# Optimization experiments

Measured on AMD Instinct MI355X. Metric: run time of the kernel, lower is better.

## Reference

```python
import jax, jax.numpy as jnp
import numpy as np

B, S, D = 256, 70, 128
NUM_NODE = 40000
N_SAMPLE = 12
ALPHA = 0.2  # leaky-relu slope


def setup_inputs() -> dict:
    key = jax.random.key(0)
    ks = jax.random.split(key, 16)
    stdv = 1.0 / np.sqrt(D)
    u = lambda k, shp: jax.random.uniform(k, shp, jnp.float32, -stdv, stdv)
    inputs = jax.random.randint(ks[0], (B, S), 0, NUM_NODE)
    adj = jax.random.randint(ks[1], (B, S, S), 0, 5)
    mask_item = jnp.ones((B, S), jnp.int32)
    item = jax.random.randint(ks[2], (B, S), 0, NUM_NODE)
    input_times = jax.random.uniform(ks[3], (B, S), jnp.float32)
    adj_all = jax.random.randint(ks[4], (NUM_NODE, N_SAMPLE), 0, NUM_NODE)
    num_w = jax.random.uniform(ks[5], (NUM_NODE, N_SAMPLE), jnp.float32)
    embedding = u(ks[6], (NUM_NODE, D))
    a0, a1, a2, a3 = (u(ks[7 + i], (D,)) for i in range(4))
    gw1 = u(ks[11], (D + 1, D))
    gw2 = u(ks[12], (D, 1))
    gw3 = u(ks[13], (2 * D, D))
    gbias = u(ks[14], (D,))
    return dict(inputs=inputs, adj=adj, mask_item=mask_item, item=item,
                input_times=input_times, adj_all=adj_all, num_w=num_w,
                embedding=embedding, a0=a0, a1=a1, a2=a2, a3=a3,
                gw1=gw1, gw2=gw2, gw3=gw3, gbias=gbias)


def reference(inputs, adj, mask_item, item, input_times, adj_all, num_w,
              embedding, a0, a1, a2, a3, gw1, gw2, gw3, gbias):
    # ---- local aggregator (4-relation GAT over session graph) ----
    h = embedding[inputs]                              # [B,S,D]
    a_in = h[:, :, None, :] * h[:, None, :, :]         # [B,S,S,D] pairwise products
    att = lambda a: jax.nn.leaky_relu(jnp.einsum('bijd,d->bij', a_in, a), ALPHA)
    e0, e1, e2, e3 = att(a0), att(a1), att(a2), att(a3)
    neg = jnp.full_like(e0, -9e15)
    alpha = jnp.where(adj == 1, e0, neg)
    alpha = jnp.where(adj == 2, e1, alpha)
    alpha = jnp.where(adj == 3, e2, alpha)
    alpha = jnp.where(adj == 4, e3, alpha)
    alpha = jax.nn.softmax(alpha, axis=-1)
    h_local = jnp.einsum('bij,bjd->bid', alpha, h)     # [B,S,D]

    # ---- global aggregator: 1-hop neighbor sampling + session-gated attention ----
    flat = inputs.reshape(-1)
    neigh = adj_all[flat].reshape(B, S, N_SAMPLE)      # sampled neighbor ids
    nw = num_w[flat].reshape(B, S, N_SAMPLE)           # neighbor co-occurrence weights
    nv = embedding[neigh]                              # [B,S,K,D]

    maskf = mask_item.astype(jnp.float32)[..., None]   # [B,S,1]
    item_emb = embedding[item] * maskf
    sess = jnp.sum(item_emb, axis=1) / jnp.sum(maskf, axis=1)   # [B,D] mean session emb
    extra = sess[:, None, None, :]                     # broadcast to [B,S,K,D]

    feat = jnp.concatenate([extra * nv, nw[..., None]], axis=-1)  # [B,S,K,D+1]
    al = jax.nn.leaky_relu(feat @ gw1, 0.2)            # [B,S,K,D]
    al = jax.nn.softmax((al @ gw2)[..., 0], axis=-1)[..., None]   # [B,S,K,1]
    nagg = jnp.sum(al * nv, axis=-2)                   # [B,S,D]

    out = jnp.concatenate([h, nagg], axis=-1) @ gw3 + gbias
    h_global = jax.nn.relu(out)                        # [B,S,D]
    # dropout_local/global = 0 (eval mode): identity
    return h_local, h_global
```

## Files before the change

kernel.cpp:

```cpp
#include <hip/hip_runtime.h>
#include <hip/hip_bf16.h>

#define B_ 256
#define S_ 70
#define D_ 128
#define NSAMP 12
#define NNODE 40000
#define HGLOB (B_ * S_ * D_)
#define IBLK 14
#define NPOS 10
#define NR2 (NPOS * NSAMP)
#define NRP 128

typedef float  f32x4 __attribute__((ext_vector_type(4)));
typedef short  s16x8 __attribute__((ext_vector_type(8)));

__device__ __forceinline__ unsigned short f2bf(float x) {
    union { float f; unsigned u; } v; v.f = x;
    return (unsigned short)((v.u + 0x7FFF + ((v.u >> 16) & 1)) >> 16);
}
__device__ __forceinline__ float bf2f(unsigned short u) {
    union { unsigned u; float f; } v; v.u = ((unsigned)u) << 16;
    return v.f;
}

__global__ __launch_bounds__(512) void prelude_kernel(const int* __restrict__ item,
                                                      const int* __restrict__ mask,
                                                      const float* __restrict__ emb,
                                                      const float* __restrict__ gw1,
                                                      const float* __restrict__ gw3,
                                                      float* __restrict__ sess,
                                                      unsigned short* __restrict__ gw1T,
                                                      unsigned short* __restrict__ gw3T,
                                                      unsigned short* __restrict__ embT) {
    if (blockIdx.x < B_) {
        __shared__ float pacc[4][D_];
        __shared__ float pm[4];
        int b = blockIdx.x;
        int d = threadIdx.x & 127, q = threadIdx.x >> 7;
        float acc = 0.f, msum = 0.f;
        for (int s = q; s < S_; s += 4) {
            int node = item[b * S_ + s];
            float m = (float)mask[b * S_ + s];
            acc += m * emb[(long)node * D_ + d];
            msum += m;
        }
        pacc[q][d] = acc;
        if (d == 0) pm[q] = msum;
        __syncthreads();
        if (q == 0) {
            float a = pacc[0][d] + pacc[1][d] + pacc[2][d] + pacc[3][d];
            float m = pm[0] + pm[1] + pm[2] + pm[3];
            sess[b * D_ + d] = a / m;
        }
    } else if (blockIdx.x < B_ + 96) {
        int idx = (blockIdx.x - B_) * 512 + threadIdx.x;
        if (idx < 128 * 128) {
            int c = idx >> 7, r = idx & 127;
            gw1T[idx] = f2bf(gw1[r * 128 + c]);
        } else if (idx < 128 * 128 + 128 * 256) {
            int j = idx - 128 * 128;
            int c = j >> 8, r = j & 255;
            gw3T[j] = f2bf(gw3[r * 128 + c]);
        }
    } else {
        long idx = (long)(blockIdx.x - (B_ + 96)) * 512 + threadIdx.x;
        if (idx < (long)NNODE * D_ / 8) {
            const float4* src = (const float4*)(emb + idx * 8);
            float4 e0 = src[0], e1 = src[1];
            s16x8 p;
            p[0] = (short)f2bf(e0.x); p[1] = (short)f2bf(e0.y);
            p[2] = (short)f2bf(e0.z); p[3] = (short)f2bf(e0.w);
            p[4] = (short)f2bf(e1.x); p[5] = (short)f2bf(e1.y);
            p[6] = (short)f2bf(e1.z); p[7] = (short)f2bf(e1.w);
            *(s16x8*)(embT + idx * 8) = p;
        }
    }
}

struct LocalSM {
    unsigned short hl[72 * 128];
    float          El[16 * 84];
    unsigned short al[16 * 104];
    int            ids[72];
};
struct GlobalSM {
    unsigned short nv[NRP * 128];
    unsigned short cat[16 * 256];
    float          spart[NRP][4];
    int            neigh[NR2];
    float          nw[NR2];
    float          score[NR2];
    float          wsm[NR2];
};

union FusedSM { LocalSM loc; GlobalSM glob; };

__global__ __launch_bounds__(256) void fused_kernel(
        const int* __restrict__ inputs, const int* __restrict__ adj,
        const int* __restrict__ adj_all, const float* __restrict__ num_w,
        const unsigned short* __restrict__ embT, const float* __restrict__ sess,
        const float* __restrict__ a0p, const float* __restrict__ a1p,
        const float* __restrict__ a2p, const float* __restrict__ a3p,
        const unsigned short* __restrict__ gw1T, const float* __restrict__ gw1,
        const float* __restrict__ gw2,
        const unsigned short* __restrict__ gw3T, const float* __restrict__ gbias,
        float* __restrict__ out) {
    __shared__ __align__(16) FusedSM smem;

    const int L = blockIdx.x;
    const int b = L / 12;
    const int r = L - b * 12;
    const int tid  = threadIdx.x;
    const int lane = tid & 63, wave = tid >> 6;
    const int l15  = lane & 15, l4 = lane >> 4;
    const s16x8 zero8 = {0, 0, 0, 0, 0, 0, 0, 0};

    if (r < 5) {
        LocalSM* P = &smem.loc;
        const int i0 = r * IBLK;

        if (tid < S_) P->ids[tid] = inputs[b * S_ + tid];
        if (tid < 32) ((s16x8*)P->hl)[70 * 16 + tid] = zero8;
        __syncthreads();

        #pragma unroll
        for (int it = 0; it < 5; ++it) {
            int idx = it * 256 + tid;
            if (idx < S_ * 16) {
                int s = idx >> 4, c8 = idx & 15;
                s16x8 p = *(const s16x8*)(embT + (long)P->ids[s] * D_ + c8 * 8);
                ((s16x8*)P->hl)[s * 16 + (c8 ^ (s & 7))] = p;
            }
        }
        __syncthreads();

        s16x8 af_all[4][4];
        {
            const float* aptr[4] = {a0p, a1p, a2p, a3p};
            int hrow = i0 + l15;
            #pragma unroll
            for (int ks = 0; ks < 4; ++ks) {
                s16x8 hf = ((s16x8*)P->hl)[hrow * 16 + ((ks * 4 + l4) ^ (hrow & 7))];
                #pragma unroll
                for (int rr = 0; rr < 4; ++rr) {
                    const float* ar = aptr[rr];
                    float4 alo = *(const float4*)(ar + ks * 32 + l4 * 8);
                    float4 ahi = *(const float4*)(ar + ks * 32 + l4 * 8 + 4);
                    s16x8 o;
                    o[0] = (short)f2bf(bf2f((unsigned short)hf[0]) * alo.x);
                    o[1] = (short)f2bf(bf2f((unsigned short)hf[1]) * alo.y);
                    o[2] = (short)f2bf(bf2f((unsigned short)hf[2]) * alo.z);
                    o[3] = (short)f2bf(bf2f((unsigned short)hf[3]) * alo.w);
                    o[4] = (short)f2bf(bf2f((unsigned short)hf[4]) * ahi.x);
                    o[5] = (short)f2bf(bf2f((unsigned short)hf[5]) * ahi.y);
                    o[6] = (short)f2bf(bf2f((unsigned short)hf[6]) * ahi.z);
                    o[7] = (short)f2bf(bf2f((unsigned short)hf[7]) * ahi.w);
                    af_all[rr][ks] = o;
                }
            }
        }

        for (int n = wave; n < 5; n += 4) {
            s16x8 bfr[4];
            int jr = n * 16 + l15;
            int jrc = jr < 72 ? jr : 71;
            #pragma unroll
            for (int ks = 0; ks < 4; ++ks)
                bfr[ks] = ((s16x8*)P->hl)[jrc * 16 + ((ks * 4 + l4) ^ (jrc & 7))];

            f32x4 ac0 = {0.f,0.f,0.f,0.f}, ac1 = {0.f,0.f,0.f,0.f};
            f32x4 ac2 = {0.f,0.f,0.f,0.f}, ac3 = {0.f,0.f,0.f,0.f};
            #pragma unroll
            for (int ks = 0; ks < 4; ++ks) {
                ac0 = __builtin_amdgcn_mfma_f32_16x16x32_bf16(af_all[0][ks], bfr[ks], ac0, 0, 0, 0);
                ac1 = __builtin_amdgcn_mfma_f32_16x16x32_bf16(af_all[1][ks], bfr[ks], ac1, 0, 0, 0);
                ac2 = __builtin_amdgcn_mfma_f32_16x16x32_bf16(af_all[2][ks], bfr[ks], ac2, 0, 0, 0);
                ac3 = __builtin_amdgcn_mfma_f32_16x16x32_bf16(af_all[3][ks], bfr[ks], ac3, 0, 0, 0);
            }

            #pragma unroll
            for (int reg = 0; reg < 4; ++reg) {
                int il = l4 * 4 + reg;
                int i  = i0 + il;
                int j  = n * 16 + l15;
                float v;
                if (j < S_) {
                    int ic = i < S_ ? i : S_ - 1;
                    int a  = adj[((long)b * S_ + ic) * S_ + j];
                    float raw = (a == 1) ? ac0[reg] : (a == 2) ? ac1[reg]
                              : (a == 3) ? ac2[reg] : (a == 4) ? ac3[reg] : 0.f;
                    v = (a >= 1 && a <= 4) ? (raw > 0.f ? raw : 0.2f * raw) : -9e15f;
                } else {
                    v = -INFINITY;
                }
                P->El[il * 84 + j] = v;
            }
        }
        __syncthreads();

        {
            int g = tid >> 4, li = tid & 15;
            float mx = -INFINITY;
            for (int j = li; j < S_; j += 16) mx = fmaxf(mx, P->El[g * 84 + j]);
            #pragma unroll
            for (int o = 1; o < 16; o <<= 1) mx = fmaxf(mx, __shfl_xor(mx, o));
            float sm = 0.f;
            for (int j = li; j < S_; j += 16) {
                float ex = __expf(P->El[g * 84 + j] - mx);
                P->El[g * 84 + j] = ex;
                sm += ex;
            }
            #pragma unroll
            for (int o = 1; o < 16; o <<= 1) sm += __shfl_xor(sm, o);
            float inv = 1.f / sm;
            for (int j = li; j < 104; j += 16)
                P->al[g * 104 + j] = (j < S_) ? f2bf(P->El[g * 84 + j] * inv) : (unsigned short)0;
        }
        __syncthreads();

        for (int n = wave; n < 8; n += 4) {
            f32x4 acc = {0.f, 0.f, 0.f, 0.f};
            int d = n * 16 + l15;
            int dchunk = d >> 3, de = d & 7;
            #pragma unroll
            for (int ks = 0; ks < 3; ++ks) {
                s16x8 afp = *(const s16x8*)(P->al + l15 * 104 + ks * 32 + l4 * 8);
                int jb = ks * 32 + l4 * 8;
                s16x8 bfp;
                #pragma unroll
                for (int e = 0; e < 8; ++e) {
                    int j = jb + e;
                    bfp[e] = (j < 72)
                        ? (short)P->hl[j * 128 + ((dchunk ^ (j & 7)) << 3) + de]
                        : (short)0;
                }
                acc = __builtin_amdgcn_mfma_f32_16x16x32_bf16(afp, bfp, acc, 0, 0, 0);
            }
            #pragma unroll
            for (int reg = 0; reg < 4; ++reg) {
                int il = l4 * 4 + reg;
                if (il < IBLK)
                    out[((long)b * S_ + (i0 + il)) * D_ + d] = acc[reg];
            }
        }
    } else {
        GlobalSM* P = &smem.glob;
        const int i0  = (r - 5) * NPOS;
        const int bs0 = b * S_ + i0;

        if (tid < NR2) {
            int p = tid / NSAMP;
            int k = tid - p * NSAMP;
            int node = inputs[bs0 + p];
            P->neigh[tid] = adj_all[node * NSAMP + k];
            P->nw[tid]    = num_w[node * NSAMP + k];
        }
        if (tid < 128) ((s16x8*)P->nv)[NR2 * 16 + tid] = zero8;
        __syncthreads();

        #pragma unroll
        for (int it = 0; it < 8; ++it) {
            int idx = it * 256 + tid;
            if (idx < NR2 * 16) {
                int row = idx >> 4, c8 = idx & 15;
                s16x8 p = *(const s16x8*)(embT + (long)P->neigh[row] * D_ + c8 * 8);
                ((s16x8*)P->nv)[row * 16 + (c8 ^ (row & 7))] = p;
            }
        }
        __syncthreads();

        s16x8 bfp[2][4];
        #pragma unroll
        for (int n = 0; n < 2; ++n) {
            int c = (wave * 2 + n) * 16 + l15;
            #pragma unroll
            for (int ks = 0; ks < 4; ++ks) {
                s16x8 g = *(const s16x8*)(gw1T + c * 128 + ks * 32 + l4 * 8);
                float4 slo = *(const float4*)(sess + b * D_ + ks * 32 + l4 * 8);
                float4 shi = *(const float4*)(sess + b * D_ + ks * 32 + l4 * 8 + 4);
                s16x8 o;
                o[0] = (short)f2bf(bf2f((unsigned short)g[0]) * slo.x);
                o[1] = (short)f2bf(bf2f((unsigned short)g[1]) * slo.y);
                o[2] = (short)f2bf(bf2f((unsigned short)g[2]) * slo.z);
                o[3] = (short)f2bf(bf2f((unsigned short)g[3]) * slo.w);
                o[4] = (short)f2bf(bf2f((unsigned short)g[4]) * shi.x);
                o[5] = (short)f2bf(bf2f((unsigned short)g[5]) * shi.y);
                o[6] = (short)f2bf(bf2f((unsigned short)g[6]) * shi.z);
                o[7] = (short)f2bf(bf2f((unsigned short)g[7]) * shi.w);
                bfp[n][ks] = o;
            }
        }
        float g128a = gw1[128 * 128 + wave * 32 + l15];
        float g128b = gw1[128 * 128 + wave * 32 + 16 + l15];
        float gw2a  = gw2[wave * 32 + l15];
        float gw2b  = gw2[wave * 32 + 16 + l15];

        for (int m = 0; m < NRP / 16; ++m) {
            int arow = m * 16 + l15;
            s16x8 af[4];
            #pragma unroll
            for (int ks = 0; ks < 4; ++ks)
                af[ks] = ((s16x8*)P->nv)[arow * 16 + ((ks * 4 + l4) ^ (arow & 7))];

            f32x4 acc0 = {0.f, 0.f, 0.f, 0.f}, acc1 = {0.f, 0.f, 0.f, 0.f};
            #pragma unroll
            for (int ks = 0; ks < 4; ++ks) {
                acc0 = __builtin_amdgcn_mfma_f32_16x16x32_bf16(af[ks], bfp[0][ks], acc0, 0, 0, 0);
                acc1 = __builtin_amdgcn_mfma_f32_16x16x32_bf16(af[ks], bfp[1][ks], acc1, 0, 0, 0);
            }

            float sp[4];
            #pragma unroll
            for (int reg = 0; reg < 4; ++reg) {
                int rr = m * 16 + l4 * 4 + reg;
                float nwv = (rr < NR2) ? P->nw[rr] : 0.f;
                float al0 = acc0[reg] + nwv * g128a;
                float al1 = acc1[reg] + nwv * g128b;
                al0 = al0 > 0.f ? al0 : 0.2f * al0;
                al1 = al1 > 0.f ? al1 : 0.2f * al1;
                sp[reg] = al0 * gw2a + al1 * gw2b;
            }
            #pragma unroll
            for (int off = 1; off < 16; off <<= 1) {
                #pragma unroll
                for (int reg = 0; reg < 4; ++reg) sp[reg] += __shfl_xor(sp[reg], off);
            }
            if (l15 == 0) {
                int rb = m * 16 + l4 * 4;
                #pragma unroll
                for (int reg = 0; reg < 4; ++reg) P->spart[rb + reg][wave] = sp[reg];
            }
        }
        __syncthreads();

        if (tid < NR2)
            P->score[tid] = P->spart[tid][0] + P->spart[tid][1] + P->spart[tid][2] + P->spart[tid][3];
        __syncthreads();

        if (tid < NPOS) {
            float mx = -1e30f;
            #pragma unroll
            for (int k = 0; k < NSAMP; ++k) mx = fmaxf(mx, P->score[tid * NSAMP + k]);
            float ex[NSAMP]; float ss = 0.f;
            #pragma unroll
            for (int k = 0; k < NSAMP; ++k) { ex[k] = __expf(P->score[tid * NSAMP + k] - mx); ss += ex[k]; }
            float inv = 1.f / ss;
            #pragma unroll
            for (int k = 0; k < NSAMP; ++k) P->wsm[tid * NSAMP + k] = ex[k] * inv;
        }
        __syncthreads();

        {
            int p  = tid >> 4;
            int c8 = tid & 15;
            if (p < NPOS) {
                float a0v[4] = {0.f,0.f,0.f,0.f}, a1v[4] = {0.f,0.f,0.f,0.f};
                #pragma unroll
                for (int k = 0; k < NSAMP; ++k) {
                    int row = p * NSAMP + k;
                    float w = P->wsm[row];
                    s16x8 nvv = ((s16x8*)P->nv)[row * 16 + (c8 ^ (row & 7))];
                    a0v[0] += w * bf2f((unsigned short)nvv[0]);
                    a0v[1] += w * bf2f((unsigned short)nvv[1]);
                    a0v[2] += w * bf2f((unsigned short)nvv[2]);
                    a0v[3] += w * bf2f((unsigned short)nvv[3]);
                    a1v[0] += w * bf2f((unsigned short)nvv[4]);
                    a1v[1] += w * bf2f((unsigned short)nvv[5]);
                    a1v[2] += w * bf2f((unsigned short)nvv[6]);
                    a1v[3] += w * bf2f((unsigned short)nvv[7]);
                }
                int node = inputs[bs0 + p];
                s16x8 ph = *(const s16x8*)(embT + (long)node * D_ + c8 * 8);
                s16x8 pa;
                pa[0]=(short)f2bf(a0v[0]); pa[1]=(short)f2bf(a0v[1]); pa[2]=(short)f2bf(a0v[2]); pa[3]=(short)f2bf(a0v[3]);
                pa[4]=(short)f2bf(a1v[0]); pa[5]=(short)f2bf(a1v[1]); pa[6]=(short)f2bf(a1v[2]); pa[7]=(short)f2bf(a1v[3]);
                ((s16x8*)P->cat)[p * 32 + ( c8       ^ (p & 7))] = ph;
                ((s16x8*)P->cat)[p * 32 + ((16 + c8) ^ (p & 7))] = pa;
            } else {
                ((s16x8*)P->cat)[p * 32 + ( c8       ^ (p & 7))] = zero8;
                ((s16x8*)P->cat)[p * 32 + ((16 + c8) ^ (p & 7))] = zero8;
            }
        }
        __syncthreads();

        {
            f32x4 acc0 = {0.f,0.f,0.f,0.f}, acc1 = {0.f,0.f,0.f,0.f};
            int arow = l15;
            int cc = wave * 32 + l15;
            #pragma unroll
            for (int ks = 0; ks < 8; ++ks) {
                s16x8 a  = ((s16x8*)P->cat)[arow * 32 + ((ks * 4 + l4) ^ (arow & 7))];
                s16x8 b0 = *(const s16x8*)(gw3T +  cc       * 256 + ks * 32 + l4 * 8);
                s16x8 b1 = *(const s16x8*)(gw3T + (cc + 16) * 256 + ks * 32 + l4 * 8);
                acc0 = __builtin_amdgcn_mfma_f32_16x16x32_bf16(a, b0, acc0, 0, 0, 0);
                acc1 = __builtin_amdgcn_mfma_f32_16x16x32_bf16(a, b1, acc1, 0, 0, 0);
            }
            float gb0 = gbias[wave * 32 + l15];
            float gb1 = gbias[wave * 32 + 16 + l15];
            #pragma unroll
            for (int reg = 0; reg < 4; ++reg) {
                int il = l4 * 4 + reg;
                if (il < NPOS) {
                    long bs = bs0 + il;
                    float o0 = acc0[reg] + gb0;
                    float o1 = acc1[reg] + gb1;
                    out[(long)HGLOB + bs * D_ + wave * 32 + l15]      = o0 > 0.f ? o0 : 0.f;
                    out[(long)HGLOB + bs * D_ + wave * 32 + 16 + l15] = o1 > 0.f ? o1 : 0.f;
                }
            }
        }
    }
}

extern "C" void kernel_launch(void* const* d_in, const int* in_sizes, int n_in,
                              void* d_out, int out_size, void* d_ws, size_t ws_size,
                              hipStream_t stream) {
    const int*   inputs  = (const int*)  d_in[0];
    const int*   adj     = (const int*)  d_in[1];
    const int*   mask    = (const int*)  d_in[2];
    const int*   item    = (const int*)  d_in[3];
    const int*   adj_all = (const int*)  d_in[5];
    const float* num_w   = (const float*)d_in[6];
    const float* emb     = (const float*)d_in[7];
    const float* a0      = (const float*)d_in[8];
    const float* a1      = (const float*)d_in[9];
    const float* a2      = (const float*)d_in[10];
    const float* a3      = (const float*)d_in[11];
    const float* gw1     = (const float*)d_in[12];
    const float* gw2     = (const float*)d_in[13];
    const float* gw3     = (const float*)d_in[14];
    const float* gbias   = (const float*)d_in[15];
    float* out = (float*)d_out;

    float*          sess = (float*)d_ws;
    unsigned short* gw1T = (unsigned short*)((char*)d_ws + 131072);
    unsigned short* gw3T = gw1T + 128 * 128;
    unsigned short* embT = gw3T + 128 * 256;

    const int embt_blocks = (NNODE * D_ / 8 + 511) / 512;
    prelude_kernel<<<B_ + 96 + embt_blocks, 512, 0, stream>>>(item, mask, emb, gw1, gw3,
                                                              sess, gw1T, gw3T, embT);
    fused_kernel<<<B_ * 12, 256, 0, stream>>>(inputs, adj, adj_all, num_w, embT, sess,
                                              a0, a1, a2, a3,
                                              gw1T, gw1, gw2, gw3T, gbias, out);
}
```

Baseline: 80.49 us.

## Add transposed LDS copy of session embeddings and pack 12 positions per global block

The local blocks now also write a transposed bf16 copy of the gathered session embeddings into LDS, so the alpha·h MFMA B-operand becomes one vector load instead of eight scalar gathers. The global path now handles 12 positions per block instead of 10, which cuts the block count from 12 to 11 per session and removes the padding rows and bounds checks from the neighbour tile. The costs are a larger local LDS footprint (zero-fill plus scattered 2-byte transposed writes, which may cause bank conflicts) and some clamped duplicate work in the last global block.

Measured after the change: 87.30 us. +8.5%, slower.

```diff
diff --git a/kernel.cpp b/kernel.cpp
--- a/kernel.cpp
+++ b/kernel.cpp
@@ -8,9 +8,10 @@
 #define NNODE 40000
 #define HGLOB (B_ * S_ * D_)
 #define IBLK 14
-#define NPOS 10
+#define NPOS 12
 #define NR2 (NPOS * NSAMP)
-#define NRP 128
+#define NROLE (5 + 6)
+#define HTS 72
 
 typedef float  f32x4 __attribute__((ext_vector_type(4)));
 typedef short  s16x8 __attribute__((ext_vector_type(8)));
@@ -80,14 +81,15 @@
 
 struct LocalSM {
     unsigned short hl[72 * 128];
+    unsigned short HT[128 * HTS + 96];
     float          El[16 * 84];
     unsigned short al[16 * 104];
     int            ids[72];
 };
 struct GlobalSM {
-    unsigned short nv[NRP * 128];
+    unsigned short nv[NR2 * 128];
     unsigned short cat[16 * 256];
-    float          spart[NRP][4];
+    float          spart[NR2][4];
     int            neigh[NR2];
     float          nw[NR2];
     float          score[NR2];
@@ -109,8 +111,8 @@
     __shared__ __align__(16) FusedSM smem;
 
     const int L = blockIdx.x;
-    const int b = L / 12;
-    const int r = L - b * 12;
+    const int b = L / NROLE;
+    const int r = L - b * NROLE;
     const int tid  = threadIdx.x;
     const int lane = tid & 63, wave = tid >> 6;
     const int l15  = lane & 15, l4 = lane >> 4;
@@ -122,6 +124,7 @@
 
         if (tid < S_) P->ids[tid] = inputs[b * S_ + tid];
         if (tid < 32) ((s16x8*)P->hl)[70 * 16 + tid] = zero8;
+        for (int c = tid; c < (128 * HTS + 96) / 8; c += 256) ((s16x8*)P->HT)[c] = zero8;
         __syncthreads();
 
         #pragma unroll
@@ -131,6 +134,9 @@
                 int s = idx >> 4, c8 = idx & 15;
                 s16x8 p = *(const s16x8*)(embT + (long)P->ids[s] * D_ + c8 * 8);
                 ((s16x8*)P->hl)[s * 16 + (c8 ^ (s & 7))] = p;
+                #pragma unroll
+                for (int e = 0; e < 8; ++e)
+                    P->HT[(c8 * 8 + e) * HTS + s] = (unsigned short)p[e];
             }
         }
         __syncthreads();
@@ -222,19 +228,10 @@
         for (int n = wave; n < 8; n += 4) {
             f32x4 acc = {0.f, 0.f, 0.f, 0.f};
             int d = n * 16 + l15;
-            int dchunk = d >> 3, de = d & 7;
             #pragma unroll
             for (int ks = 0; ks < 3; ++ks) {
                 s16x8 afp = *(const s16x8*)(P->al + l15 * 104 + ks * 32 + l4 * 8);
-                int jb = ks * 32 + l4 * 8;
-                s16x8 bfp;
-                #pragma unroll
-                for (int e = 0; e < 8; ++e) {
-                    int j = jb + e;
-                    bfp[e] = (j < 72)
-                        ? (short)P->hl[j * 128 + ((dchunk ^ (j & 7)) << 3) + de]
-                        : (short)0;
-                }
+                s16x8 bfp = *(const s16x8*)(P->HT + d * HTS + ks * 32 + l4 * 8);
                 acc = __builtin_amdgcn_mfma_f32_16x16x32_bf16(afp, bfp, acc, 0, 0, 0);
             }
             #pragma unroll
@@ -252,21 +249,19 @@
         if (tid < NR2) {
             int p = tid / NSAMP;
             int k = tid - p * NSAMP;
-            int node = inputs[bs0 + p];
+            int pos = i0 + p; if (pos >= S_) pos = S_ - 1;
+            int node = inputs[b * S_ + pos];
             P->neigh[tid] = adj_all[node * NSAMP + k];
             P->nw[tid]    = num_w[node * NSAMP + k];
         }
-        if (tid < 128) ((s16x8*)P->nv)[NR2 * 16 + tid] = zero8;
         __syncthreads();
 
         #pragma unroll
-        for (int it = 0; it < 8; ++it) {
+        for (int it = 0; it < 9; ++it) {
             int idx = it * 256 + tid;
-            if (idx < NR2 * 16) {
-                int row = idx >> 4, c8 = idx & 15;
-                s16x8 p = *(const s16x8*)(embT + (long)P->neigh[row] * D_ + c8 * 8);
-                ((s16x8*)P->nv)[row * 16 + (c8 ^ (row & 7))] = p;
-            }
+            int row = idx >> 4, c8 = idx & 15;
+            s16x8 p = *(const s16x8*)(embT + (long)P->neigh[row] * D_ + c8 * 8);
+            ((s16x8*)P->nv)[row * 16 + (c8 ^ (row & 7))] = p;
         }
         __syncthreads();
 
@@ -296,7 +291,7 @@
         float gw2a  = gw2[wave * 32 + l15];
         float gw2b  = gw2[wave * 32 + 16 + l15];
 
-        for (int m = 0; m < NRP / 16; ++m) {
+        for (int m = 0; m < NR2 / 16; ++m) {
             int arow = m * 16 + l15;
             s16x8 af[4];
             #pragma unroll
@@ -314,7 +309,7 @@
             #pragma unroll
             for (int reg = 0; reg < 4; ++reg) {
                 int rr = m * 16 + l4 * 4 + reg;
-                float nwv = (rr < NR2) ? P->nw[rr] : 0.f;
+                float nwv = P->nw[rr];
                 float al0 = acc0[reg] + nwv * g128a;
                 float al1 = acc1[reg] + nwv * g128b;
                 al0 = al0 > 0.f ? al0 : 0.2f * al0;
@@ -370,7 +365,8 @@
                     a1v[2] += w * bf2f((unsigned short)nvv[6]);
                     a1v[3] += w * bf2f((unsigned short)nvv[7]);
                 }
-                int node = inputs[bs0 + p];
+                int pos = i0 + p; if (pos >= S_) pos = S_ - 1;
+                int node = inputs[b * S_ + pos];
                 s16x8 ph = *(const s16x8*)(embT + (long)node * D_ + c8 * 8);
                 s16x8 pa;
                 pa[0]=(short)f2bf(a0v[0]); pa[1]=(short)f2bf(a0v[1]); pa[2]=(short)f2bf(a0v[2]); pa[3]=(short)f2bf(a0v[3]);
@@ -401,7 +397,7 @@
             #pragma unroll
             for (int reg = 0; reg < 4; ++reg) {
                 int il = l4 * 4 + reg;
-                if (il < NPOS) {
+                if (il < NPOS && i0 + il < S_) {
                     long bs = bs0 + il;
                     float o0 = acc0[reg] + gb0;
                     float o1 = acc1[reg] + gb1;
@@ -441,7 +437,7 @@
     const int embt_blocks = (NNODE * D_ / 8 + 511) / 512;
     prelude_kernel<<<B_ + 96 + embt_blocks, 512, 0, stream>>>(item, mask, emb, gw1, gw3,
                                                               sess, gw1T, gw3T, embT);
-    fused_kernel<<<B_ * 12, 256, 0, stream>>>(inputs, adj, adj_all, num_w, embT, sess,
-                                              a0, a1, a2, a3,
-                                              gw1T, gw1, gw2, gw3T, gbias, out);
+    fused_kernel<<<B_ * NROLE, 256, 0, stream>>>(inputs, adj, adj_all, num_w, embT, sess,
+                                                 a0, a1, a2, a3,
+                                                 gw1T, gw1, gw2, gw3T, gbias, out);
 }
```
